# Kernel tuning notes

Measured on AMD Instinct MI355X. Metric: run time of the kernel, lower is better.

## Reference

```python
import jax, jax.numpy as jnp
import numpy as np

N = 100000      # nodes
E = 800000      # directed edges (avg in-degree 8)
FIN = 2         # node features: [type, requests]
C = 32          # embedding_size (per-head out channels)
H = 4           # heads
HC = H * C      # 128
L = 3           # extra conv layers after conv1
D1, D2 = 128, 64
NL = 15         # num_locations
BN_EPS = 1e-5


def _tconv(x, src, dst, ea, qw, qb, kw, kb, vw, vb, ew, skw, skb, bw):
    """PyG TransformerConv with heads=H, concat=True, beta=True, edge_dim."""
    n = x.shape[0]
    q = (x @ qw.T + qb).reshape(n, H, C)
    k = (x @ kw.T + kb).reshape(n, H, C)
    v = (x @ vw.T + vb).reshape(n, H, C)
    e = (ea @ ew.T).reshape(-1, H, C)                     # [E,H,C], lin_edge has no bias
    ke = k[src] + e
    alpha = (q[dst] * ke).sum(-1) / jnp.sqrt(jnp.float32(C))   # [E,H]
    # scatter-softmax over incoming edges of each destination node
    amax = jax.ops.segment_max(alpha, dst, num_segments=n)     # [N,H]
    ex = jnp.exp(alpha - amax[dst])
    denom = jax.ops.segment_sum(ex, dst, num_segments=n)
    attn = ex / jnp.where(denom > 0, denom, 1.0)[dst]
    msg = (v[src] + e) * attn[..., None]                       # [E,H,C]
    out = jax.ops.segment_sum(msg, dst, num_segments=n).reshape(n, HC)
    skip = x @ skw.T + skb                                     # root transform
    beta = jax.nn.sigmoid(jnp.concatenate([out, skip, out - skip], -1) @ bw.T)  # [N,1]
    return beta * skip + (1.0 - beta) * out


def _bn(x, g, b):
    # BatchNorm1d with batch statistics (biased variance), as in torch training math
    mu = x.mean(0)
    var = ((x - mu) ** 2).mean(0)
    return (x - mu) / jnp.sqrt(var + BN_EPS) * g + b


def _forward(node_type, requests, latency, active_mask, edge_index, P):
    (q1_w, q1_b, k1_w, k1_b, v1_w, v1_b, e1_w, skip1_w, skip1_b, beta1_w,
     transf1_w, transf1_b, bn1_g, bn1_b,
     qL_w, qL_b, kL_w, kL_b, vL_w, vL_b, eL_w, skipL_w, skipL_b, betaL_w,
     transfL_w, transfL_b, bnL_g, bnL_b,
     lin1_w, lin1_b, lin2_w, lin2_b, rem_w, rem_b, addp_w, addp_b) = P
    src, dst = edge_index[0], edge_index[1]
    ea = latency[:, None]                                  # [E,1]
    x = jnp.stack([node_type, requests], 1)                # [N,2]
    x = _tconv(x, src, dst, ea, q1_w, q1_b, k1_w, k1_b, v1_w, v1_b,
               e1_w, skip1_w, skip1_b, beta1_w)
    x = _bn(jax.nn.relu(x @ transf1_w.T + transf1_b), bn1_g, bn1_b)
    for i in range(L):
        x = _tconv(x, src, dst, ea, qL_w[i], qL_b[i], kL_w[i], kL_b[i], vL_w[i], vL_b[i],
                   eL_w[i], skipL_w[i], skipL_b[i], betaL_w[i])
        x = _bn(jax.nn.relu(x @ transfL_w[i].T + transfL_b[i]), bnL_g[i], bnL_b[i])
    x = jax.nn.relu(x @ lin1_w.T + lin1_b)                 # dropout(p=0.8) is eval no-op
    x = jax.nn.relu(x @ lin2_w.T + lin2_b)                 # [N,D2]
    mask = active_mask
    head = mask[:NL]
    rm_head = jnp.where(head == 0.0, -jnp.inf, jnp.where(jnp.isneginf(head), 0.0, head))
    remove_mask = mask.at[:NL].set(rm_head)
    removed_logits = (x @ rem_w.T + rem_b)[:, 0] + remove_mask   # [N]
    k1, k2 = jax.random.split(jax.random.key(42))
    action1 = jax.random.categorical(k1, removed_logits)
    mask2 = mask.at[action1].set(0.0)
    proj = jnp.tanh(x[action1] @ addp_w.T + addp_b)              # [D2]
    new_logits = x @ proj + mask2                                # [N]
    action2 = jax.random.categorical(k2, new_logits)
    return removed_logits, new_logits, action1, action2


def setup_inputs() -> dict:
    key = jax.random.key(0)
    ks = iter(jax.random.split(key, 80))
    def nrm(shape, s=0.1):
        return jax.random.normal(next(ks), shape, jnp.float32) * s
    inp = {
        "node_type": jax.random.uniform(next(ks), (N,), jnp.float32),
        "requests": jax.random.uniform(next(ks), (N,), jnp.float32),
        "latency": jax.random.uniform(next(ks), (E,), jnp.float32),
        "active_mask": jnp.zeros((N,), jnp.float32),
        "edge_index": jax.random.randint(next(ks), (2, E), 0, N, dtype=jnp.int32),
        "q1_w": nrm((HC, FIN)), "q1_b": jnp.zeros((HC,)),
        "k1_w": nrm((HC, FIN)), "k1_b": jnp.zeros((HC,)),
        "v1_w": nrm((HC, FIN)), "v1_b": jnp.zeros((HC,)),
        "e1_w": nrm((HC, 1)),
        "skip1_w": nrm((HC, FIN)), "skip1_b": jnp.zeros((HC,)),
        "beta1_w": nrm((1, 3 * HC)),
        "transf1_w": nrm((C, HC)), "transf1_b": jnp.zeros((C,)),
        "bn1_g": jnp.ones((C,)), "bn1_b": jnp.zeros((C,)),
        "qL_w": nrm((L, HC, C)), "qL_b": jnp.zeros((L, HC)),
        "kL_w": nrm((L, HC, C)), "kL_b": jnp.zeros((L, HC)),
        "vL_w": nrm((L, HC, C)), "vL_b": jnp.zeros((L, HC)),
        "eL_w": nrm((L, HC, 1)),
        "skipL_w": nrm((L, HC, C)), "skipL_b": jnp.zeros((L, HC)),
        "betaL_w": nrm((L, 1, 3 * HC)),
        "transfL_w": nrm((L, C, HC)), "transfL_b": jnp.zeros((L, C)),
        "bnL_g": jnp.ones((L, C)), "bnL_b": jnp.zeros((L, C)),
        "lin1_w": nrm((D1, C)), "lin1_b": jnp.zeros((D1,)),
        "lin2_w": nrm((D2, D1)), "lin2_b": jnp.zeros((D2,)),
        "rem_w": nrm((1, D2)), "rem_b": jnp.zeros((1,)),
        "addp_w": nrm((D2, D2)), "addp_b": jnp.zeros((D2,)),
    }
    return inp


def reference(node_type, requests, latency, active_mask, edge_index,
              q1_w, q1_b, k1_w, k1_b, v1_w, v1_b, e1_w, skip1_w, skip1_b, beta1_w,
              transf1_w, transf1_b, bn1_g, bn1_b,
              qL_w, qL_b, kL_w, kL_b, vL_w, vL_b, eL_w, skipL_w, skipL_b, betaL_w,
              transfL_w, transfL_b, bnL_g, bnL_b,
              lin1_w, lin1_b, lin2_w, lin2_b, rem_w, rem_b, addp_w, addp_b):
    P = (q1_w, q1_b, k1_w, k1_b, v1_w, v1_b, e1_w, skip1_w, skip1_b, beta1_w,
         transf1_w, transf1_b, bn1_g, bn1_b,
         qL_w, qL_b, kL_w, kL_b, vL_w, vL_b, eL_w, skipL_w, skipL_b, betaL_w,
         transfL_w, transfL_b, bnL_g, bnL_b,
         lin1_w, lin1_b, lin2_w, lin2_b, rem_w, rem_b, addp_w, addp_b)
    rl, nl, a1, a2 = _forward(node_type, requests, latency, active_mask, edge_index, P)
    log_probs = jnp.stack([jax.nn.log_softmax(rl)[a1], jax.nn.log_softmax(nl)[a2]])
    logits = jnp.stack([rl, nl])      # [2,N]
    actions = jnp.stack([a1, a2])     # [2]
    return logits, actions, log_probs
```

## Files before the change

### kernel.cpp

```cpp
#include <hip/hip_runtime.h>
#include <hip/hip_bf16.h>
#include <math.h>
#include <stdint.h>
#include <limits.h>

#define NN 100000
#define NE 800000
#define PB 512
#define NDB 512
#define NEGBIG (-1e30f)

typedef __hip_bfloat16 bf16;

__device__ __forceinline__ float bf2f(unsigned short u)
{
  union { unsigned v; float f; } x; x.v = ((unsigned)u) << 16; return x.f;
}
__device__ __forceinline__ unsigned short f2bf(float f)
{
  bf16 h = __float2bfloat16(f);
  return *reinterpret_cast<unsigned short*>(&h);
}
__device__ __forceinline__ unsigned pk2(float a, float b)
{
  return (unsigned)f2bf(a) | ((unsigned)f2bf(b) << 16);
}

__device__ __forceinline__ uint2 tf_dev(unsigned k0, unsigned k1, unsigned x0, unsigned x1)
{
  const unsigned ks2 = k0 ^ k1 ^ 0x1BD11BDAu;
#define TFR(r) { x0 += x1; x1 = (x1 << r) | (x1 >> (32 - r)); x1 ^= x0; }
  x0 += k0; x1 += k1;
  TFR(13) TFR(15) TFR(26) TFR(6)
  x0 += k1; x1 += ks2 + 1u;
  TFR(17) TFR(29) TFR(16) TFR(24)
  x0 += ks2; x1 += k0 + 2u;
  TFR(13) TFR(15) TFR(26) TFR(6)
  x0 += k0; x1 += k1 + 3u;
  TFR(17) TFR(29) TFR(16) TFR(24)
  x0 += k1; x1 += ks2 + 4u;
  TFR(13) TFR(15) TFR(26) TFR(6)
  x0 += ks2; x1 += k0 + 5u;
#undef TFR
  return make_uint2(x0, x1);
}

static void tf_host(unsigned k0, unsigned k1, unsigned x0, unsigned x1,
                    unsigned* o0, unsigned* o1)
{
  const unsigned ks2 = k0 ^ k1 ^ 0x1BD11BDAu;
#define TFR(r) { x0 += x1; x1 = (x1 << r) | (x1 >> (32 - r)); x1 ^= x0; }
  x0 += k0; x1 += k1;
  TFR(13) TFR(15) TFR(26) TFR(6)
  x0 += k1; x1 += ks2 + 1u;
  TFR(17) TFR(29) TFR(16) TFR(24)
  x0 += ks2; x1 += k0 + 2u;
  TFR(13) TFR(15) TFR(26) TFR(6)
  x0 += k0; x1 += k1 + 3u;
  TFR(17) TFR(29) TFR(16) TFR(24)
  x0 += k1; x1 += ks2 + 4u;
  TFR(13) TFR(15) TFR(26) TFR(6)
  x0 += ks2; x1 += k0 + 5u;
#undef TFR
  *o0 = x0; *o1 = x1;
}

__device__ __forceinline__ float gumbel_of(unsigned ka, unsigned kb, int i)
{
  uint2 c = tf_dev(ka, kb, 0u, (unsigned)i);
  unsigned bits = c.x ^ c.y;
  float f = __uint_as_float((bits >> 9) | 0x3f800000u) - 1.0f;
  const float TINYF = 1.17549435e-38f;
  float u = fmaxf(TINYF, f + TINYF);
  return -logf(-logf(u));
}

__global__ __launch_bounds__(256) void k_zero2(int* __restrict__ a, int* __restrict__ b)
{
  int i = blockIdx.x * 256 + threadIdx.x;
  if (i < NN) { a[i] = 0; b[i] = 0; }
}

__global__ __launch_bounds__(256) void k_hist(const int* __restrict__ edst, int* __restrict__ deg)
{
  int e = blockIdx.x * 256 + threadIdx.x;
  if (e < NE) atomicAdd(&deg[edst[e]], 1);
}

__global__ __launch_bounds__(1024) void k_scan(const int* __restrict__ deg, int* __restrict__ rowptr)
{
  __shared__ int wsum[16];
  __shared__ int chtot;
  const int t = threadIdx.x;
  const int lane = t & 63;
  const int wv = t >> 6;
  int carry = 0;
  for (int base = 0; base < NN; base += 4096) {
    int i0 = base + t * 4;
    int d0 = 0, d1 = 0, d2 = 0, d3 = 0;
    if (i0 + 3 < NN) { int4 dd = *(const int4*)(deg + i0); d0 = dd.x; d1 = dd.y; d2 = dd.z; d3 = dd.w; }
    else {
      if (i0     < NN) d0 = deg[i0];
      if (i0 + 1 < NN) d1 = deg[i0 + 1];
      if (i0 + 2 < NN) d2 = deg[i0 + 2];
      if (i0 + 3 < NN) d3 = deg[i0 + 3];
    }
    int tsum = d0 + d1 + d2 + d3;
    int sc = tsum;
    #pragma unroll
    for (int off = 1; off < 64; off <<= 1) { int o = __shfl_up(sc, off); if (lane >= off) sc += o; }
    if (lane == 63) wsum[wv] = sc;
    __syncthreads();
    if (wv == 0 && lane < 16) {
      int wval = wsum[lane];
      int wsc = wval;
      #pragma unroll
      for (int off = 1; off < 16; off <<= 1) { int o = __shfl_up(wsc, off); if (lane >= off) wsc += o; }
      if (lane == 15) chtot = wsc;
      wsum[lane] = wsc - wval;
    }
    __syncthreads();
    int excl = carry + wsum[wv] + (sc - tsum);
    if (i0     < NN) rowptr[i0]     = excl;
    if (i0 + 1 < NN) rowptr[i0 + 1] = excl + d0;
    if (i0 + 2 < NN) rowptr[i0 + 2] = excl + d0 + d1;
    if (i0 + 3 < NN) rowptr[i0 + 3] = excl + d0 + d1 + d2;
    carry += chtot;
    __syncthreads();
  }
  if (t == 0) rowptr[NN] = carry;
}

__global__ __launch_bounds__(256) void k_scatter(
    const int* __restrict__ esrc, const int* __restrict__ edst,
    const float* __restrict__ lat, const int* __restrict__ rowptr,
    int* __restrict__ fill, int2* __restrict__ csr)
{
  int e = blockIdx.x * 256 + threadIdx.x;
  if (e >= NE) return;
  int d = edst[e];
  int pos = rowptr[d] + atomicAdd(&fill[d], 1);
  csr[pos] = make_int2(esrc[e], __float_as_int(lat[e]));
}

__global__ __launch_bounds__(256) void k_qkvs_first(
    const float* __restrict__ nt, const float* __restrict__ rq,
    const float* __restrict__ qw, const float* __restrict__ qbv,
    const float* __restrict__ kw, const float* __restrict__ kbv,
    const float* __restrict__ vw, const float* __restrict__ vbv,
    const float* __restrict__ sw, const float* __restrict__ sbv,
    unsigned* __restrict__ q, unsigned short* __restrict__ kv, unsigned* __restrict__ sk)
{
  int idx = blockIdx.x * 256 + threadIdx.x;
  if (idx >= NN * 64) return;
  int n = idx >> 6, l = idx & 63;
  int j0 = 2 * l, j1 = 2 * l + 1;
  float a = nt[n], b = rq[n];
  float q0 = (a * qw[2 * j0] + b * qw[2 * j0 + 1]) + qbv[j0];
  float q1 = (a * qw[2 * j1] + b * qw[2 * j1 + 1]) + qbv[j1];
  q[idx] = pk2(q0, q1);
  ushort4 kvo;
  kvo.x = f2bf((a * kw[2 * j0] + b * kw[2 * j0 + 1]) + kbv[j0]);
  kvo.y = f2bf((a * kw[2 * j1] + b * kw[2 * j1 + 1]) + kbv[j1]);
  kvo.z = f2bf((a * vw[2 * j0] + b * vw[2 * j0 + 1]) + vbv[j0]);
  kvo.w = f2bf((a * vw[2 * j1] + b * vw[2 * j1 + 1]) + vbv[j1]);
  ((ushort4*)kv)[idx] = kvo;
  float s0 = (a * sw[2 * j0] + b * sw[2 * j0 + 1]) + sbv[j0];
  float s1 = (a * sw[2 * j1] + b * sw[2 * j1 + 1]) + sbv[j1];
  sk[idx] = pk2(s0, s1);
}

#define QP 36
#define WP 33
__global__ __launch_bounds__(256) void k_qkvs3(
    const float* __restrict__ yb, const float* __restrict__ stats,
    const float* __restrict__ bng, const float* __restrict__ bnb,
    const float* __restrict__ wq, const float* __restrict__ bq,
    const float* __restrict__ wk, const float* __restrict__ bk,
    const float* __restrict__ wv, const float* __restrict__ bv,
    const float* __restrict__ wsk, const float* __restrict__ bsk,
    unsigned* __restrict__ oq, unsigned short* __restrict__ okv, unsigned* __restrict__ osk)
{
  __shared__ __align__(16) float xs[64 * QP];
  __shared__ __align__(16) float Wl[2 * 128 * WP];

  const int t = threadIdx.x;
  const int nq = t & 15;
  const int chq = t >> 4;
  const int y = blockIdx.y;

  if (y == 1) {
    for (int idx = t; idx < 128 * 32; idx += 256) {
      int c = idx >> 5, k = idx & 31;
      Wl[c * WP + k] = wk[idx];
      Wl[128 * WP + c * WP + k] = wv[idx];
    }
  } else {
    const float* W = (y == 0) ? wq : wsk;
    for (int idx = t; idx < 128 * 32; idx += 256) {
      int c = idx >> 5, k = idx & 31;
      Wl[c * WP + k] = W[idx];
    }
  }

  const int ch0 = (t & 7) * 4;
  float sc[4], sh[4];
  #pragma unroll
  for (int c = 0; c < 4; ++c) {
    int ch = ch0 + c;
    float rsig = 1.0f / stats[32 + ch];
    sc[c] = bng[ch] * rsig;
    sh[c] = bnb[ch] - stats[ch] * sc[c];
  }

  const int ntiles = (NN + 63) / 64;
  for (int tile = blockIdx.x; tile < ntiles; tile += gridDim.x) {
    const int base = tile * 64;
    __syncthreads();
    #pragma unroll
    for (int rep = 0; rep < 2; ++rep) {
      int f = t + rep * 256;
      int n = f >> 3, kq = f & 7;
      int gn = base + n;
      if (gn >= NN) gn = NN - 1;
      float4 v = *(const float4*)(yb + (size_t)gn * 32 + kq * 4);
      v.x = fmaf(v.x, sc[0], sh[0]);
      v.y = fmaf(v.y, sc[1], sh[1]);
      v.z = fmaf(v.z, sc[2], sh[2]);
      v.w = fmaf(v.w, sc[3], sh[3]);
      *(float4*)(xs + n * QP + kq * 4) = v;
    }
    __syncthreads();

    if (y == 1) {
      float ak[4][8], av[4][8];
      #pragma unroll
      for (int s = 0; s < 4; ++s)
        #pragma unroll
        for (int j = 0; j < 8; ++j) { ak[s][j] = bk[chq * 8 + j]; av[s][j] = bv[chq * 8 + j]; }
      #pragma unroll 4
      for (int k2 = 0; k2 < 16; ++k2) {
        const int k = 2 * k2;
        float2 xv[4];
        #pragma unroll
        for (int s = 0; s < 4; ++s) xv[s] = *(const float2*)(xs + (nq + 16 * s) * QP + k);
        #pragma unroll
        for (int j = 0; j < 8; ++j) {
          float2 wk2 = *(const float2*)(Wl + (chq * 8 + j) * WP + k);
          float2 wv2 = *(const float2*)(Wl + 128 * WP + (chq * 8 + j) * WP + k);
          #pragma unroll
          for (int s = 0; s < 4; ++s) {
            ak[s][j] = fmaf(xv[s].x, wk2.x, ak[s][j]);
            ak[s][j] = fmaf(xv[s].y, wk2.y, ak[s][j]);
            av[s][j] = fmaf(xv[s].x, wv2.x, av[s][j]);
            av[s][j] = fmaf(xv[s].y, wv2.y, av[s][j]);
          }
        }
      }
      #pragma unroll
      for (int s = 0; s < 4; ++s) {
        int node = base + nq + 16 * s;
        if (node < NN) {
          uint4 A, B;
          A.x = pk2(ak[s][0], ak[s][1]); A.y = pk2(av[s][0], av[s][1]);
          A.z = pk2(ak[s][2], ak[s][3]); A.w = pk2(av[s][2], av[s][3]);
          B.x = pk2(ak[s][4], ak[s][5]); B.y = pk2(av[s][4], av[s][5]);
          B.z = pk2(ak[s][6], ak[s][7]); B.w = pk2(av[s][6], av[s][7]);
          unsigned short* dst = okv + (size_t)node * 256 + chq * 16;
          *(uint4*)dst = A;
          *(uint4*)(dst + 8) = B;
        }
      }
    } else {
      const float* B = (y == 0) ? bq : bsk;
      unsigned* Of = (y == 0) ? oq : osk;
      float acc[4][8];
      #pragma unroll
      for (int s = 0; s < 4; ++s)
        #pragma unroll
        for (int j = 0; j < 8; ++j) acc[s][j] = B[chq * 8 + j];
      #pragma unroll 4
      for (int k2 = 0; k2 < 16; ++k2) {
        const int k = 2 * k2;
        float2 xv[4];
        #pragma unroll
        for (int s = 0; s < 4; ++s) xv[s] = *(const float2*)(xs + (nq + 16 * s) * QP + k);
        #pragma unroll
        for (int j = 0; j < 8; ++j) {
          float2 w2 = *(const float2*)(Wl + (chq * 8 + j) * WP + k);
          #pragma unroll
          for (int s = 0; s < 4; ++s) {
            acc[s][j] = fmaf(xv[s].x, w2.x, acc[s][j]);
            acc[s][j] = fmaf(xv[s].y, w2.y, acc[s][j]);
          }
        }
      }
      #pragma unroll
      for (int s = 0; s < 4; ++s) {
        int node = base + nq + 16 * s;
        if (node < NN) {
          uint4 Q;
          Q.x = pk2(acc[s][0], acc[s][1]);
          Q.y = pk2(acc[s][2], acc[s][3]);
          Q.z = pk2(acc[s][4], acc[s][5]);
          Q.w = pk2(acc[s][6], acc[s][7]);
          *(uint4*)(Of + (size_t)node * 64 + chq * 4) = Q;
        }
      }
    }
  }
}

__global__ __launch_bounds__(256) void k_lin1d(
    const float* __restrict__ yb, const float* __restrict__ stats,
    const float* __restrict__ bng, const float* __restrict__ bnb,
    const float* __restrict__ W, const float* __restrict__ B, unsigned* __restrict__ O)
{
  __shared__ __align__(16) float xs[64 * QP];
  __shared__ __align__(16) float Wl[128 * WP];
  const int t = threadIdx.x;
  const int nq = t & 15;
  const int chq = t >> 4;
  for (int idx = t; idx < 128 * 32; idx += 256) {
    int c = idx >> 5, k = idx & 31;
    Wl[c * WP + k] = W[idx];
  }
  const int ch0 = (t & 7) * 4;
  float sc[4], sh[4];
  #pragma unroll
  for (int c = 0; c < 4; ++c) {
    int ch = ch0 + c;
    float rsig = 1.0f / stats[32 + ch];
    sc[c] = bng[ch] * rsig;
    sh[c] = bnb[ch] - stats[ch] * sc[c];
  }
  const int ntiles = (NN + 63) / 64;
  for (int tile = blockIdx.x; tile < ntiles; tile += gridDim.x) {
    const int base = tile * 64;
    __syncthreads();
    #pragma unroll
    for (int rep = 0; rep < 2; ++rep) {
      int f = t + rep * 256;
      int n = f >> 3, kq = f & 7;
      int gn = base + n;
      if (gn >= NN) gn = NN - 1;
      float4 v = *(const float4*)(yb + (size_t)gn * 32 + kq * 4);
      v.x = fmaf(v.x, sc[0], sh[0]);
      v.y = fmaf(v.y, sc[1], sh[1]);
      v.z = fmaf(v.z, sc[2], sh[2]);
      v.w = fmaf(v.w, sc[3], sh[3]);
      *(float4*)(xs + n * QP + kq * 4) = v;
    }
    __syncthreads();
    float acc[4][8];
    #pragma unroll
    for (int s = 0; s < 4; ++s)
      #pragma unroll
      for (int j = 0; j < 8; ++j) acc[s][j] = B[chq * 8 + j];
    #pragma unroll 4
    for (int k2 = 0; k2 < 16; ++k2) {
      const int k = 2 * k2;
      float2 xv[4];
      #pragma unroll
      for (int s = 0; s < 4; ++s) xv[s] = *(const float2*)(xs + (nq + 16 * s) * QP + k);
      #pragma unroll
      for (int j = 0; j < 8; ++j) {
        float2 w2 = *(const float2*)(Wl + (chq * 8 + j) * WP + k);
        #pragma unroll
        for (int s = 0; s < 4; ++s) {
          acc[s][j] = fmaf(xv[s].x, w2.x, acc[s][j]);
          acc[s][j] = fmaf(xv[s].y, w2.y, acc[s][j]);
        }
      }
    }
    #pragma unroll
    for (int s = 0; s < 4; ++s) {
      int node = base + nq + 16 * s;
      if (node < NN) {
        uint4 P;
        P.x = pk2(fmaxf(acc[s][0], 0.f), fmaxf(acc[s][1], 0.f));
        P.y = pk2(fmaxf(acc[s][2], 0.f), fmaxf(acc[s][3], 0.f));
        P.z = pk2(fmaxf(acc[s][4], 0.f), fmaxf(acc[s][5], 0.f));
        P.w = pk2(fmaxf(acc[s][6], 0.f), fmaxf(acc[s][7], 0.f));
        *(uint4*)(O + (size_t)node * 64 + chq * 4) = P;
      }
    }
  }
}

#define XPITCH 132
#define WPITCH 130
template<int COUT, bool STATS, bool REM>
__global__ __launch_bounds__(256) void k_dense(
    const unsigned* __restrict__ xin, const float* __restrict__ W,
    const float* __restrict__ bias, float* __restrict__ out,
    double* __restrict__ psum, double* __restrict__ psq,
    const float* __restrict__ rw, const float* __restrict__ rb,
    const float* __restrict__ amask, float* __restrict__ rl)
{
  constexpr int JB = COUT / 16;
  __shared__ __align__(16) float xs[64 * XPITCH];
  __shared__ float Ws[COUT * WPITCH];
  __shared__ float rem_lds[REM ? 16 * 64 : 1];

  const int t = threadIdx.x;
  const int nq = t & 15;
  const int chq = t >> 4;

  for (int idx = t; idx < COUT * 128; idx += 256) {
    int c = idx >> 7, k = idx & 127;
    Ws[c * WPITCH + k] = W[idx];
  }
  float bj[JB];
  float rwj[REM ? JB : 1];
  #pragma unroll
  for (int j = 0; j < JB; ++j) {
    bj[j] = bias[chq * JB + j];
    if (REM) rwj[j] = rw[chq * JB + j];
  }
  double sd[STATS ? JB : 1], sq[STATS ? JB : 1];
  if (STATS) {
    #pragma unroll
    for (int j = 0; j < JB; ++j) { sd[j] = 0.0; sq[j] = 0.0; }
  }

  const uint4* xin4 = (const uint4*)xin;
  const int ntiles = (NN + 63) / 64;
  for (int tile = blockIdx.x; tile < ntiles; tile += gridDim.x) {
    const int base = tile * 64;
    __syncthreads();
    #pragma unroll
    for (int r = 0; r < 4; ++r) {
      int f = t + r * 256;
      int n = f >> 4, kq = f & 15;
      int gn = base + n;
      if (gn >= NN) gn = NN - 1;
      uint4 v = xin4[(size_t)gn * 16 + kq];
      float* d = xs + n * XPITCH + kq * 8;
      float4 lo, hi;
      lo.x = bf2f((unsigned short)(v.x & 0xffffu)); lo.y = bf2f((unsigned short)(v.x >> 16));
      lo.z = bf2f((unsigned short)(v.y & 0xffffu)); lo.w = bf2f((unsigned short)(v.y >> 16));
      hi.x = bf2f((unsigned short)(v.z & 0xffffu)); hi.y = bf2f((unsigned short)(v.z >> 16));
      hi.z = bf2f((unsigned short)(v.w & 0xffffu)); hi.w = bf2f((unsigned short)(v.w >> 16));
      *(float4*)d = lo;
      *(float4*)(d + 4) = hi;
    }
    __syncthreads();

    float acc[4][JB];
    #pragma unroll
    for (int s = 0; s < 4; ++s)
      #pragma unroll
      for (int j = 0; j < JB; ++j) acc[s][j] = bj[j];

    #pragma unroll 8
    for (int k2 = 0; k2 < 64; ++k2) {
      const int k = 2 * k2;
      float2 xv[4];
      #pragma unroll
      for (int s = 0; s < 4; ++s)
        xv[s] = *(const float2*)(xs + (nq + 16 * s) * XPITCH + k);
      float2 wv[JB];
      #pragma unroll
      for (int j = 0; j < JB; ++j)
        wv[j] = *(const float2*)(Ws + (chq * JB + j) * WPITCH + k);
      #pragma unroll
      for (int s = 0; s < 4; ++s)
        #pragma unroll
        for (int j = 0; j < JB; ++j) {
          acc[s][j] = fmaf(xv[s].x, wv[j].x, acc[s][j]);
          acc[s][j] = fmaf(xv[s].y, wv[j].y, acc[s][j]);
        }
    }

    #pragma unroll
    for (int s = 0; s < 4; ++s) {
      const int node = base + nq + 16 * s;
      const bool ok = node < NN;
      #pragma unroll
      for (int j = 0; j < JB; ++j) acc[s][j] = fmaxf(acc[s][j], 0.f);
      if (ok) {
        if (COUT == 32) {
          *(float2*)(out + (size_t)node * 32 + chq * 2) = make_float2(acc[s][0], acc[s][1]);
        } else {
          *(float4*)(out + (size_t)node * 64 + chq * 4) =
              make_float4(acc[s][0], acc[s][1], acc[s][2], acc[s][3]);
        }
      }
      if (STATS && ok) {
        #pragma unroll
        for (int j = 0; j < JB; ++j) {
          sd[j] += (double)acc[s][j];
          sq[j] += (double)acc[s][j] * (double)acc[s][j];
        }
      }
      if (REM) {
        float p = 0.f;
        #pragma unroll
        for (int j = 0; j < JB; ++j) p = fmaf(acc[s][j], rwj[j], p);
        rem_lds[chq * 64 + nq + 16 * s] = p;
      }
    }

    if (REM) {
      __syncthreads();
      if (t < 64) {
        int node = base + t;
        if (node < NN) {
          float v = rb[0];
          #pragma unroll
          for (int c = 0; c < 16; ++c) v += rem_lds[c * 64 + t];
          float mv = amask[node];
          float mterm;
          if (node < 15) mterm = (mv == 0.f) ? -INFINITY : ((mv == -INFINITY) ? 0.f : mv);
          else mterm = mv;
          rl[node] = fmaxf(v + mterm, NEGBIG);
        }
      }
    }
  }

  if (STATS) {
    __shared__ double sred[256 * 2];
    __syncthreads();
    #pragma unroll
    for (int j = 0; j < JB; ++j) { sred[t * 2 + j] = sd[j]; }
    __syncthreads();
    if (t < 32) {
      int cq = t >> 1, j = t & 1;
      double a = 0.0;
      #pragma unroll
      for (int n = 0; n < 16; ++n) a += sred[(cq * 16 + n) * 2 + j];
      psum[blockIdx.x * 32 + t] = a;
    }
    __syncthreads();
    #pragma unroll
    for (int j = 0; j < JB; ++j) { sred[t * 2 + j] = sq[j]; }
    __syncthreads();
    if (t < 32) {
      int cq = t >> 1, j = t & 1;
      double a = 0.0;
      #pragma unroll
      for (int n = 0; n < 16; ++n) a += sred[(cq * 16 + n) * 2 + j];
      psq[blockIdx.x * 32 + t] = a;
    }
  }
}

__global__ __launch_bounds__(1024) void k_stats2(
    const double* __restrict__ psum, const double* __restrict__ psq, float* __restrict__ stats)
{
  const int t = threadIdx.x;
  const int ch = t & 31;
  const int chunk = t >> 5;
  double s = 0.0, q = 0.0;
  for (int b = chunk; b < NDB; b += 32) { s += psum[b * 32 + ch]; q += psq[b * 32 + ch]; }
  __shared__ double rs[1024];
  __shared__ double rq[1024];
  rs[t] = s; rq[t] = q;
  __syncthreads();
  for (int off = 16; off > 0; off >>= 1) {
    if (chunk < off) { rs[t] += rs[t + off * 32]; rq[t] += rq[t + off * 32]; }
    __syncthreads();
  }
  if (t < 32) {
    double mu = rs[t] / (double)NN;
    double var = rq[t] / (double)NN - mu * mu;
    if (var < 0.0) var = 0.0;
    stats[t] = (float)mu;
    stats[32 + t] = sqrtf((float)var + 1e-5f);
  }
}

__global__ __launch_bounds__(256) void k_attn(
    const unsigned* __restrict__ qb, const unsigned short* __restrict__ kvb,
    unsigned* __restrict__ skh,
    const int* __restrict__ rowptr, const int2* __restrict__ csr,
    const float* __restrict__ ew, const float* __restrict__ bw)
{
  const int wid = (blockIdx.x * 256 + threadIdx.x) >> 6;
  const int lane = threadIdx.x & 63;
  if (wid >= NN) return;
  const unsigned qu = qb[(size_t)wid * 64 + lane];
  const float qx = bf2f((unsigned short)(qu & 0xffffu));
  const float qy = bf2f((unsigned short)(qu >> 16));
  const float2 ew2 = ((const float2*)ew)[lane];
  const ushort4* kvp = (const ushort4*)kvb;
  const int p0 = rowptr[wid], p1 = rowptr[wid + 1];

  float s = 0.f, accx = 0.f, accy = 0.f;
  const float iscale = 0.17677669529663689f;

#define EDGE_BODY(cc, kv) {                                            \
    float lat = __int_as_float(cc.y);                                  \
    float e0 = lat * ew2.x, e1 = lat * ew2.y;                          \
    float kx = bf2f(kv.x) + e0, ky = bf2f(kv.y) + e1;                  \
    float part = qx * kx + qy * ky;                                    \
    part += __shfl_xor(part, 1);                                       \
    part += __shfl_xor(part, 2);                                       \
    part += __shfl_xor(part, 4);                                       \
    part += __shfl_xor(part, 8);                                       \
    float pt = __expf(part * iscale);                                  \
    float vx = bf2f(kv.z) + e0, vy = bf2f(kv.w) + e1;                  \
    s += pt;                                                           \
    accx = fmaf(pt, vx, accx);                                         \
    accy = fmaf(pt, vy, accy); }

  int p = p0;
  for (; p + 7 < p1; p += 8) {
    int2 c0 = csr[p],     c1 = csr[p + 1], c2 = csr[p + 2], c3 = csr[p + 3];
    int2 c4 = csr[p + 4], c5 = csr[p + 5], c6 = csr[p + 6], c7 = csr[p + 7];
    ushort4 kv0 = kvp[(size_t)c0.x * 64 + lane];
    ushort4 kv1 = kvp[(size_t)c1.x * 64 + lane];
    ushort4 kv2 = kvp[(size_t)c2.x * 64 + lane];
    ushort4 kv3 = kvp[(size_t)c3.x * 64 + lane];
    ushort4 kv4 = kvp[(size_t)c4.x * 64 + lane];
    ushort4 kv5 = kvp[(size_t)c5.x * 64 + lane];
    ushort4 kv6 = kvp[(size_t)c6.x * 64 + lane];
    ushort4 kv7 = kvp[(size_t)c7.x * 64 + lane];
    EDGE_BODY(c0, kv0)
    EDGE_BODY(c1, kv1)
    EDGE_BODY(c2, kv2)
    EDGE_BODY(c3, kv3)
    EDGE_BODY(c4, kv4)
    EDGE_BODY(c5, kv5)
    EDGE_BODY(c6, kv6)
    EDGE_BODY(c7, kv7)
  }
  for (; p + 3 < p1; p += 4) {
    int2 c0 = csr[p], c1 = csr[p + 1], c2 = csr[p + 2], c3 = csr[p + 3];
    ushort4 kv0 = kvp[(size_t)c0.x * 64 + lane];
    ushort4 kv1 = kvp[(size_t)c1.x * 64 + lane];
    ushort4 kv2 = kvp[(size_t)c2.x * 64 + lane];
    ushort4 kv3 = kvp[(size_t)c3.x * 64 + lane];
    EDGE_BODY(c0, kv0)
    EDGE_BODY(c1, kv1)
    EDGE_BODY(c2, kv2)
    EDGE_BODY(c3, kv3)
  }
  for (; p < p1; ++p) {
    int2 c0 = csr[p];
    ushort4 kv0 = kvp[(size_t)c0.x * 64 + lane];
    EDGE_BODY(c0, kv0)
  }
#undef EDGE_BODY

  float inv = (s > 0.f) ? (1.0f / s) : 1.0f;
  float ox = accx * inv, oy = accy * inv;

  unsigned su = skh[(size_t)wid * 64 + lane];
  float skx = bf2f((unsigned short)(su & 0xffffu));
  float sky = bf2f((unsigned short)(su >> 16));
  const float2* bw2 = (const float2*)bw;
  float2 b1 = bw2[lane], b2 = bw2[64 + lane], b3 = bw2[128 + lane];
  float part = b1.x * ox + b1.y * oy + b2.x * skx + b2.y * sky
             + b3.x * (ox - skx) + b3.y * (oy - sky);
  #pragma unroll
  for (int off = 1; off < 64; off <<= 1) part += __shfl_xor(part, off);
  float beta = 1.f / (1.f + __expf(-part));
  float hx = beta * skx + (1.f - beta) * ox;
  float hy = beta * sky + (1.f - beta) * oy;
  skh[(size_t)wid * 64 + lane] = pk2(hx, hy);
}

__global__ __launch_bounds__(256) void k_pass(
    const float* __restrict__ lg,
    float* __restrict__ pm, float* __restrict__ ps, float* __restrict__ pg, int* __restrict__ pidx,
    unsigned ka, unsigned kb)
{
  float m = -INFINITY, s = 0.f, g = -INFINITY; int gi = INT_MAX; bool hg = false;
  for (int i = blockIdx.x * 256 + threadIdx.x; i < NN; i += gridDim.x * 256) {
    float v = lg[i];
    if (v > m) { s = (m == -INFINITY) ? 1.f : fmaf(s, expf(m - v), 1.f); m = v; }
    else if (v != -INFINITY) s += expf(v - m);
    float tot = v + gumbel_of(ka, kb, i);
    if (!hg || tot > g || (tot == g && i < gi)) { g = tot; gi = i; hg = true; }
  }
  __shared__ float sm[256], ss[256], sg[256]; __shared__ int si[256];
  int t = threadIdx.x;
  sm[t] = m; ss[t] = s; sg[t] = g; si[t] = gi;
  __syncthreads();
  for (int off = 128; off > 0; off >>= 1) {
    if (t < off) {
      float m2 = sm[t + off], s2 = ss[t + off];
      float M = fmaxf(sm[t], m2);
      float sn = 0.f;
      if (M != -INFINITY) {
        if (sm[t] != -INFINITY) sn += ss[t] * expf(sm[t] - M);
        if (m2 != -INFINITY) sn += s2 * expf(m2 - M);
      }
      sm[t] = M; ss[t] = sn;
      float g2 = sg[t + off]; int i2 = si[t + off];
      if (g2 > sg[t] || (g2 == sg[t] && i2 < si[t])) { sg[t] = g2; si[t] = i2; }
    }
    __syncthreads();
  }
  if (t == 0) { pm[blockIdx.x] = sm[0]; ps[blockIdx.x] = ss[0]; pg[blockIdx.x] = sg[0]; pidx[blockIdx.x] = si[0]; }
}

__global__ __launch_bounds__(PB) void k_choose(
    const float* __restrict__ lg,
    const float* __restrict__ pm, const float* __restrict__ ps,
    const float* __restrict__ pg, const int* __restrict__ pidx,
    float* __restrict__ act_out, float* __restrict__ lp_out, int* __restrict__ a_scr,
    const float* __restrict__ xf, const float* __restrict__ aw,
    const float* __restrict__ ab, float* __restrict__ proj)
{
  __shared__ float sm[PB], ss[PB], sg[PB]; __shared__ int si[PB];
  __shared__ float xs2[64];
  int t = threadIdx.x;
  sm[t] = pm[t]; ss[t] = ps[t]; sg[t] = pg[t]; si[t] = pidx[t];
  __syncthreads();
  for (int off = PB / 2; off > 0; off >>= 1) {
    if (t < off) {
      float m2 = sm[t + off], s2 = ss[t + off];
      float M = fmaxf(sm[t], m2);
      float sn = 0.f;
      if (M != -INFINITY) {
        if (sm[t] != -INFINITY) sn += ss[t] * expf(sm[t] - M);
        if (m2 != -INFINITY) sn += s2 * expf(m2 - M);
      }
      sm[t] = M; ss[t] = sn;
      float g2 = sg[t + off]; int i2 = si[t + off];
      if (g2 > sg[t] || (g2 == sg[t] && i2 < si[t])) { sg[t] = g2; si[t] = i2; }
    }
    __syncthreads();
  }
  if (t == 0) {
    int a = si[0];
    a_scr[0] = a;
    act_out[0] = (float)a;
    lp_out[0] = (lg[a] - sm[0]) - logf(ss[0]);
  }
  if (aw != nullptr) {
    __syncthreads();
    int a = si[0];
    if (t < 64) xs2[t] = xf[(size_t)a * 64 + t];
    __syncthreads();
    if (t < 64) {
      float acc = 0.f;
      #pragma unroll
      for (int i = 0; i < 64; ++i) acc = fmaf(xs2[i], aw[t * 64 + i], acc);
      proj[t] = tanhf(acc + ab[t]);
    }
  }
}

__global__ __launch_bounds__(256) void k_nl(
    const float* __restrict__ xf, const float* __restrict__ proj,
    const float* __restrict__ amask, const int* __restrict__ a1p, float* __restrict__ nl)
{
  int wid = (blockIdx.x * 256 + threadIdx.x) >> 6;
  int lane = threadIdx.x & 63;
  if (wid >= NN) return;
  float part = xf[(size_t)wid * 64 + lane] * proj[lane];
  #pragma unroll
  for (int off = 1; off < 64; off <<= 1) part += __shfl_xor(part, off);
  if (lane == 0) {
    int a1 = a1p[0];
    float mv = (wid == a1) ? 0.f : amask[wid];
    nl[wid] = fmaxf(part + mv, NEGBIG);
  }
}

extern "C" void kernel_launch(void* const* d_in, const int* in_sizes, int n_in,
                              void* d_out, int out_size, void* d_ws, size_t ws_size,
                              hipStream_t stream)
{
  (void)in_sizes; (void)n_in; (void)out_size; (void)ws_size;

  const float* node_type = (const float*)d_in[0];
  const float* requests  = (const float*)d_in[1];
  const float* latency   = (const float*)d_in[2];
  const float* amask     = (const float*)d_in[3];
  const int*   eidx      = (const int*)d_in[4];
  const int* esrc = eidx;
  const int* edst = eidx + NE;

  const float* q1_w = (const float*)d_in[5];  const float* q1_b = (const float*)d_in[6];
  const float* k1_w = (const float*)d_in[7];  const float* k1_b = (const float*)d_in[8];
  const float* v1_w = (const float*)d_in[9];  const float* v1_b = (const float*)d_in[10];
  const float* e1_w = (const float*)d_in[11];
  const float* sk1_w = (const float*)d_in[12]; const float* sk1_b = (const float*)d_in[13];
  const float* be1_w = (const float*)d_in[14];
  const float* tf1_w = (const float*)d_in[15]; const float* tf1_b = (const float*)d_in[16];
  const float* bn1_g = (const float*)d_in[17]; const float* bn1_b = (const float*)d_in[18];
  const float* qL_w = (const float*)d_in[19]; const float* qL_b = (const float*)d_in[20];
  const float* kL_w = (const float*)d_in[21]; const float* kL_b = (const float*)d_in[22];
  const float* vL_w = (const float*)d_in[23]; const float* vL_b = (const float*)d_in[24];
  const float* eL_w = (const float*)d_in[25];
  const float* skL_w = (const float*)d_in[26]; const float* skL_b = (const float*)d_in[27];
  const float* beL_w = (const float*)d_in[28];
  const float* tfL_w = (const float*)d_in[29]; const float* tfL_b = (const float*)d_in[30];
  const float* bnL_g = (const float*)d_in[31]; const float* bnL_b = (const float*)d_in[32];
  const float* l1_w = (const float*)d_in[33]; const float* l1_b = (const float*)d_in[34];
  const float* l2_w = (const float*)d_in[35]; const float* l2_b = (const float*)d_in[36];
  const float* rem_w = (const float*)d_in[37]; const float* rem_b = (const float*)d_in[38];
  const float* ap_w = (const float*)d_in[39]; const float* ap_b = (const float*)d_in[40];

  char* ws = (char*)d_ws;
  size_t off = 0;
  auto alloc = [&](size_t bytes) -> void* {
    void* p = ws + off;
    off += (bytes + 255) & ~(size_t)255;
    return p;
  };
  unsigned* qbuf = (unsigned*)alloc((size_t)NN * 64 * 4);
  unsigned short* kvbuf = (unsigned short*)alloc((size_t)NN * 256 * 2);
  unsigned* skb = (unsigned*)alloc((size_t)NN * 64 * 4);
  float* yb   = (float*)alloc((size_t)NN * 32 * 4);
  int*   rowptr = (int*)alloc((size_t)(NN + 1) * 4);
  int*   deg    = (int*)alloc((size_t)NN * 4);
  int*   fill   = (int*)alloc((size_t)NN * 4);
  int2*  csr    = (int2*)alloc((size_t)NE * 8);
  double* psum = (double*)alloc((size_t)NDB * 32 * 8);
  double* psq  = (double*)alloc((size_t)NDB * 32 * 8);
  float* stats = (float*)alloc(64 * 4);
  float* pm = (float*)alloc(PB * 4);
  float* ps = (float*)alloc(PB * 4);
  float* pg = (float*)alloc(PB * 4);
  int*   pidx = (int*)alloc(PB * 4);
  float* proj = (float*)alloc(64 * 4);
  int*   a_scr = (int*)alloc(2 * 4);
  unsigned* y1 = skb;
  float* xf = (float*)kvbuf;

  unsigned k1a, k1b, k2a, k2b;
  tf_host(0u, 42u, 0u, 0u, &k1a, &k1b);
  tf_host(0u, 42u, 0u, 1u, &k2a, &k2b);

  float* dout = (float*)d_out;

  k_zero2<<<(NN + 255) / 256, 256, 0, stream>>>(deg, fill);
  k_hist<<<(NE + 255) / 256, 256, 0, stream>>>(edst, deg);
  k_scan<<<1, 1024, 0, stream>>>(deg, rowptr);
  k_scatter<<<(NE + 255) / 256, 256, 0, stream>>>(esrc, edst, latency, rowptr, fill, csr);

  k_qkvs_first<<<(NN * 64 + 255) / 256, 256, 0, stream>>>(
      node_type, requests, q1_w, q1_b, k1_w, k1_b, v1_w, v1_b, sk1_w, sk1_b,
      qbuf, kvbuf, skb);
  k_attn<<<NN / 4, 256, 0, stream>>>(qbuf, kvbuf, skb, rowptr, csr, e1_w, be1_w);
  k_dense<32, true, false><<<NDB, 256, 0, stream>>>(skb, tf1_w, tf1_b, yb, psum, psq,
                                                    nullptr, nullptr, nullptr, nullptr);
  k_stats2<<<1, 1024, 0, stream>>>(psum, psq, stats);

  for (int i = 0; i < 3; ++i) {
    const float* g = (i == 0) ? bn1_g : bnL_g + (i - 1) * 32;
    const float* b = (i == 0) ? bn1_b : bnL_b + (i - 1) * 32;
    k_qkvs3<<<dim3(NDB, 3), 256, 0, stream>>>(
        yb, stats, g, b,
        qL_w + i * 4096, qL_b + i * 128,
        kL_w + i * 4096, kL_b + i * 128,
        vL_w + i * 4096, vL_b + i * 128,
        skL_w + i * 4096, skL_b + i * 128,
        qbuf, kvbuf, skb);
    k_attn<<<NN / 4, 256, 0, stream>>>(qbuf, kvbuf, skb, rowptr, csr,
                                       eL_w + i * 128, beL_w + i * 384);
    k_dense<32, true, false><<<NDB, 256, 0, stream>>>(skb, tfL_w + i * 4096, tfL_b + i * 32,
                                                      yb, psum, psq,
                                                      nullptr, nullptr, nullptr, nullptr);
    k_stats2<<<1, 1024, 0, stream>>>(psum, psq, stats);
  }

  k_lin1d<<<NDB, 256, 0, stream>>>(yb, stats, bnL_g + 2 * 32, bnL_b + 2 * 32, l1_w, l1_b, y1);
  k_dense<64, false, true><<<NDB, 256, 0, stream>>>(y1, l2_w, l2_b, xf, nullptr, nullptr,
                                                    rem_w, rem_b, amask, dout);

  k_pass<<<PB, 256, 0, stream>>>(dout, pm, ps, pg, pidx, k1a, k1b);
  k_choose<<<1, PB, 0, stream>>>(dout, pm, ps, pg, pidx,
                                 dout + 2 * NN, dout + 2 * NN + 2, a_scr,
                                 xf, ap_w, ap_b, proj);
  k_nl<<<NN / 4, 256, 0, stream>>>(xf, proj, amask, a_scr, dout + NN);
  k_pass<<<PB, 256, 0, stream>>>(dout + NN, pm, ps, pg, pidx, k2a, k2b);
  k_choose<<<1, PB, 0, stream>>>(dout + NN, pm, ps, pg, pidx,
                                 dout + 2 * NN + 1, dout + 2 * NN + 3, a_scr + 1,
                                 nullptr, nullptr, nullptr, nullptr);
}
```

Measured before the change: 836.4 us.

## Split attention wavefront into two half-waves processing alternate edges with wider loads

The attention kernel now has each 32-lane half of a wavefront handle a different incoming edge, with each lane loading 16 bytes (4 channels of k and v) instead of 8. This halves the number of serial edge iterations per node and shortens the per-edge head reduction to three shuffles. The two halves are combined with a cross-half shuffle at the end. Odd edge counts are handled with a masked tail step, and only the low half writes the output.

Result: slower. 895.0 us (+7.0%).

```diff
diff --git a/kernel.cpp b/kernel.cpp
--- a/kernel.cpp
+++ b/kernel.cpp
@@ -25,6 +25,8 @@
 {
   return (unsigned)f2bf(a) | ((unsigned)f2bf(b) << 16);
 }
+#define LO16(u) ((unsigned short)((u) & 0xffffu))
+#define HI16(u) ((unsigned short)((u) >> 16))
 
 __device__ __forceinline__ uint2 tf_dev(unsigned k0, unsigned k1, unsigned x0, unsigned x1)
 {
@@ -438,10 +440,10 @@
       uint4 v = xin4[(size_t)gn * 16 + kq];
       float* d = xs + n * XPITCH + kq * 8;
       float4 lo, hi;
-      lo.x = bf2f((unsigned short)(v.x & 0xffffu)); lo.y = bf2f((unsigned short)(v.x >> 16));
-      lo.z = bf2f((unsigned short)(v.y & 0xffffu)); lo.w = bf2f((unsigned short)(v.y >> 16));
-      hi.x = bf2f((unsigned short)(v.z & 0xffffu)); hi.y = bf2f((unsigned short)(v.z >> 16));
-      hi.z = bf2f((unsigned short)(v.w & 0xffffu)); hi.w = bf2f((unsigned short)(v.w >> 16));
+      lo.x = bf2f(LO16(v.x)); lo.y = bf2f(HI16(v.x));
+      lo.z = bf2f(LO16(v.y)); lo.w = bf2f(HI16(v.y));
+      hi.x = bf2f(LO16(v.z)); hi.y = bf2f(HI16(v.z));
+      hi.z = bf2f(LO16(v.w)); hi.w = bf2f(HI16(v.w));
       *(float4*)d = lo;
       *(float4*)(d + 4) = hi;
     }
@@ -580,87 +582,113 @@
 {
   const int wid = (blockIdx.x * 256 + threadIdx.x) >> 6;
   const int lane = threadIdx.x & 63;
+  const int jl = lane & 31;
+  const int hf = lane >> 5;
   if (wid >= NN) return;
-  const unsigned qu = qb[(size_t)wid * 64 + lane];
-  const float qx = bf2f((unsigned short)(qu & 0xffffu));
-  const float qy = bf2f((unsigned short)(qu >> 16));
-  const float2 ew2 = ((const float2*)ew)[lane];
-  const ushort4* kvp = (const ushort4*)kvb;
+
+  uint2 qu = *(const uint2*)(qb + (size_t)wid * 64 + 2 * jl);
+  const float q0 = bf2f(LO16(qu.x)), q1 = bf2f(HI16(qu.x));
+  const float q2 = bf2f(LO16(qu.y)), q3 = bf2f(HI16(qu.y));
+  float4 ew4 = *(const float4*)(ew + 4 * jl);
+  const uint4* kvp4 = (const uint4*)kvb;
   const int p0 = rowptr[wid], p1 = rowptr[wid + 1];
 
-  float s = 0.f, accx = 0.f, accy = 0.f;
+  float s = 0.f, a0 = 0.f, a1 = 0.f, a2 = 0.f, a3 = 0.f;
   const float iscale = 0.17677669529663689f;
 
-#define EDGE_BODY(cc, kv) {                                            \
-    float lat = __int_as_float(cc.y);                                  \
-    float e0 = lat * ew2.x, e1 = lat * ew2.y;                          \
-    float kx = bf2f(kv.x) + e0, ky = bf2f(kv.y) + e1;                  \
-    float part = qx * kx + qy * ky;                                    \
-    part += __shfl_xor(part, 1);                                       \
-    part += __shfl_xor(part, 2);                                       \
-    part += __shfl_xor(part, 4);                                       \
-    part += __shfl_xor(part, 8);                                       \
-    float pt = __expf(part * iscale);                                  \
-    float vx = bf2f(kv.z) + e0, vy = bf2f(kv.w) + e1;                  \
-    s += pt;                                                           \
-    accx = fmaf(pt, vx, accx);                                         \
-    accy = fmaf(pt, vy, accy); }
+#define STEP(c, kv) {                                                   \
+    float lat = __int_as_float((c).y);                                  \
+    float e0 = lat * ew4.x, e1 = lat * ew4.y;                           \
+    float e2 = lat * ew4.z, e3 = lat * ew4.w;                           \
+    float part = (bf2f(LO16((kv).x)) + e0) * q0                         \
+               + (bf2f(HI16((kv).x)) + e1) * q1                         \
+               + (bf2f(LO16((kv).z)) + e2) * q2                         \
+               + (bf2f(HI16((kv).z)) + e3) * q3;                        \
+    part += __shfl_xor(part, 1);                                        \
+    part += __shfl_xor(part, 2);                                        \
+    part += __shfl_xor(part, 4);                                        \
+    float pt = __expf(part * iscale);                                   \
+    s += pt;                                                            \
+    a0 = fmaf(pt, bf2f(LO16((kv).y)) + e0, a0);                         \
+    a1 = fmaf(pt, bf2f(HI16((kv).y)) + e1, a1);                         \
+    a2 = fmaf(pt, bf2f(LO16((kv).w)) + e2, a2);                         \
+    a3 = fmaf(pt, bf2f(HI16((kv).w)) + e3, a3); }
+
+#define STEPV(c, kv, vf) {                                              \
+    float lat = __int_as_float((c).y);                                  \
+    float e0 = lat * ew4.x, e1 = lat * ew4.y;                           \
+    float e2 = lat * ew4.z, e3 = lat * ew4.w;                           \
+    float part = (bf2f(LO16((kv).x)) + e0) * q0                         \
+               + (bf2f(HI16((kv).x)) + e1) * q1                         \
+               + (bf2f(LO16((kv).z)) + e2) * q2                         \
+               + (bf2f(HI16((kv).z)) + e3) * q3;                        \
+    part += __shfl_xor(part, 1);                                        \
+    part += __shfl_xor(part, 2);                                        \
+    part += __shfl_xor(part, 4);                                        \
+    float pt = __expf(part * iscale) * (vf);                            \
+    s += pt;                                                            \
+    a0 = fmaf(pt, bf2f(LO16((kv).y)) + e0, a0);                         \
+    a1 = fmaf(pt, bf2f(HI16((kv).y)) + e1, a1);                         \
+    a2 = fmaf(pt, bf2f(LO16((kv).w)) + e2, a2);                         \
+    a3 = fmaf(pt, bf2f(HI16((kv).w)) + e3, a3); }
 
   int p = p0;
   for (; p + 7 < p1; p += 8) {
-    int2 c0 = csr[p],     c1 = csr[p + 1], c2 = csr[p + 2], c3 = csr[p + 3];
-    int2 c4 = csr[p + 4], c5 = csr[p + 5], c6 = csr[p + 6], c7 = csr[p + 7];
-    ushort4 kv0 = kvp[(size_t)c0.x * 64 + lane];
-    ushort4 kv1 = kvp[(size_t)c1.x * 64 + lane];
-    ushort4 kv2 = kvp[(size_t)c2.x * 64 + lane];
-    ushort4 kv3 = kvp[(size_t)c3.x * 64 + lane];
-    ushort4 kv4 = kvp[(size_t)c4.x * 64 + lane];
-    ushort4 kv5 = kvp[(size_t)c5.x * 64 + lane];
-    ushort4 kv6 = kvp[(size_t)c6.x * 64 + lane];
-    ushort4 kv7 = kvp[(size_t)c7.x * 64 + lane];
-    EDGE_BODY(c0, kv0)
-    EDGE_BODY(c1, kv1)
-    EDGE_BODY(c2, kv2)
-    EDGE_BODY(c3, kv3)
-    EDGE_BODY(c4, kv4)
-    EDGE_BODY(c5, kv5)
-    EDGE_BODY(c6, kv6)
-    EDGE_BODY(c7, kv7)
-  }
-  for (; p + 3 < p1; p += 4) {
-    int2 c0 = csr[p], c1 = csr[p + 1], c2 = csr[p + 2], c3 = csr[p + 3];
-    ushort4 kv0 = kvp[(size_t)c0.x * 64 + lane];
-    ushort4 kv1 = kvp[(size_t)c1.x * 64 + lane];
-    ushort4 kv2 = kvp[(size_t)c2.x * 64 + lane];
-    ushort4 kv3 = kvp[(size_t)c3.x * 64 + lane];
-    EDGE_BODY(c0, kv0)
-    EDGE_BODY(c1, kv1)
-    EDGE_BODY(c2, kv2)
-    EDGE_BODY(c3, kv3)
-  }
-  for (; p < p1; ++p) {
-    int2 c0 = csr[p];
-    ushort4 kv0 = kvp[(size_t)c0.x * 64 + lane];
-    EDGE_BODY(c0, kv0)
-  }
-#undef EDGE_BODY
+    int2 c0 = csr[p + hf];
+    int2 c1 = csr[p + 2 + hf];
+    int2 c2 = csr[p + 4 + hf];
+    int2 c3 = csr[p + 6 + hf];
+    uint4 kv0 = kvp4[(size_t)c0.x * 32 + jl];
+    uint4 kv1 = kvp4[(size_t)c1.x * 32 + jl];
+    uint4 kv2 = kvp4[(size_t)c2.x * 32 + jl];
+    uint4 kv3 = kvp4[(size_t)c3.x * 32 + jl];
+    STEP(c0, kv0)
+    STEP(c1, kv1)
+    STEP(c2, kv2)
+    STEP(c3, kv3)
+  }
+  for (; p < p1; p += 2) {
+    int ei = p + hf;
+    int pe = (ei < p1) ? ei : p;
+    float vf = (ei < p1) ? 1.f : 0.f;
+    int2 c = csr[pe];
+    uint4 kv = kvp4[(size_t)c.x * 32 + jl];
+    STEPV(c, kv, vf)
+  }
+#undef STEP
+#undef STEPV
+
+  s  += __shfl_xor(s, 32);
+  a0 += __shfl_xor(a0, 32);
+  a1 += __shfl_xor(a1, 32);
+  a2 += __shfl_xor(a2, 32);
+  a3 += __shfl_xor(a3, 32);
 
   float inv = (s > 0.f) ? (1.0f / s) : 1.0f;
-  float ox = accx * inv, oy = accy * inv;
-
-  unsigned su = skh[(size_t)wid * 64 + lane];
-  float skx = bf2f((unsigned short)(su & 0xffffu));
-  float sky = bf2f((unsigned short)(su >> 16));
-  const float2* bw2 = (const float2*)bw;
-  float2 b1 = bw2[lane], b2 = bw2[64 + lane], b3 = bw2[128 + lane];
-  float part = b1.x * ox + b1.y * oy + b2.x * skx + b2.y * sky
-             + b3.x * (ox - skx) + b3.y * (oy - sky);
-  #pragma unroll
-  for (int off = 1; off < 64; off <<= 1) part += __shfl_xor(part, off);
+  float o0 = a0 * inv, o1 = a1 * inv, o2 = a2 * inv, o3 = a3 * inv;
+
+  uint2 su = *(const uint2*)(skh + (size_t)wid * 64 + 2 * jl);
+  float sk0 = bf2f(LO16(su.x)), sk1 = bf2f(HI16(su.x));
+  float sk2 = bf2f(LO16(su.y)), sk3 = bf2f(HI16(su.y));
+  float4 b1 = *(const float4*)(bw + 4 * jl);
+  float4 b2 = *(const float4*)(bw + 128 + 4 * jl);
+  float4 b3 = *(const float4*)(bw + 256 + 4 * jl);
+  float part = b1.x * o0 + b1.y * o1 + b1.z * o2 + b1.w * o3
+             + b2.x * sk0 + b2.y * sk1 + b2.z * sk2 + b2.w * sk3
+             + b3.x * (o0 - sk0) + b3.y * (o1 - sk1)
+             + b3.z * (o2 - sk2) + b3.w * (o3 - sk3);
+  part += __shfl_xor(part, 1);
+  part += __shfl_xor(part, 2);
+  part += __shfl_xor(part, 4);
+  part += __shfl_xor(part, 8);
+  part += __shfl_xor(part, 16);
   float beta = 1.f / (1.f + __expf(-part));
-  float hx = beta * skx + (1.f - beta) * ox;
-  float hy = beta * sky + (1.f - beta) * oy;
-  skh[(size_t)wid * 64 + lane] = pk2(hx, hy);
+  float h0 = beta * sk0 + (1.f - beta) * o0;
+  float h1 = beta * sk1 + (1.f - beta) * o1;
+  float h2 = beta * sk2 + (1.f - beta) * o2;
+  float h3 = beta * sk3 + (1.f - beta) * o3;
+  if (hf == 0)
+    *(uint2*)(skh + (size_t)wid * 64 + 2 * jl) = make_uint2(pk2(h0, h1), pk2(h2, h3));
 }
 
 __global__ __launch_bounds__(256) void k_pass(
```
